# Kernel tuning notes

Measured on AMD Instinct MI355X. Metric: run time of the kernel, lower is better.

## Reference

```python
import jax, jax.numpy as jnp
import numpy as np

DIM = 1024
N_HEADS = 16
HEAD_DIM = 64
SEQ = 2048
BATCH = 2


def setup_inputs() -> dict:
    key = jax.random.key(0)
    ks = jax.random.split(key, 7)
    scale = 1.0 / np.sqrt(DIM)
    return {
        "q": jax.random.normal(ks[0], (BATCH, SEQ, DIM), dtype=jnp.float32),
        "k": jax.random.normal(ks[1], (BATCH, SEQ, DIM), dtype=jnp.float32),
        "v": jax.random.normal(ks[2], (BATCH, SEQ, DIM), dtype=jnp.float32),
        "wq": jax.random.normal(ks[3], (DIM, DIM), dtype=jnp.float32) * scale,
        "wk": jax.random.normal(ks[4], (DIM, DIM), dtype=jnp.float32) * scale,
        "wv": jax.random.normal(ks[5], (DIM, DIM), dtype=jnp.float32) * scale,
        "wo": jax.random.normal(ks[6], (DIM, DIM), dtype=jnp.float32) * scale,
    }


def reference(q, k, v, wq, wk, wv, wo):
    B, S, D = q.shape
    # Linear layers: y = x @ W.T (torch nn.Linear convention)
    qh = (q @ wq.T).reshape(B, S, N_HEADS, HEAD_DIM).transpose(0, 2, 1, 3)  # [B,H,S,hd]
    kh = (k @ wk.T).reshape(B, S, N_HEADS, HEAD_DIM).transpose(0, 2, 1, 3)
    vh = (v @ wv.T).reshape(B, S, N_HEADS, HEAD_DIM).transpose(0, 2, 1, 3)
    score = jnp.einsum('bhqd,bhkd->bhqk', qh, kh) / jnp.sqrt(jnp.float32(HEAD_DIM))
    # causal mask: upper triangle (j > i) set to -inf
    causal = jnp.tril(jnp.ones((S, S), dtype=bool))
    score = jnp.where(causal[None, None], score, -jnp.inf)
    attn = jax.nn.softmax(score, axis=-1)
    out = jnp.einsum('bhqk,bhkd->bhqd', attn, vh)  # [B,H,S,hd]
    out = out.transpose(0, 2, 1, 3).reshape(B, S, D)
    return out @ wo.T
```

## Files before the change

### kernel.cpp

```cpp
#include <hip/hip_runtime.h>

typedef unsigned short u16;
typedef unsigned int   u32;
typedef __bf16 bf16x8 __attribute__((ext_vector_type(8)));
typedef float  f32x4  __attribute__((ext_vector_type(4)));
typedef unsigned short u16x4 __attribute__((ext_vector_type(4)));
typedef unsigned short u16x8 __attribute__((ext_vector_type(8)));
typedef unsigned int   u32x2 __attribute__((ext_vector_type(2)));
typedef unsigned int   u32x4 __attribute__((ext_vector_type(4)));

#define DIM   1024
#define SEQ   2048
#define NH    16
#define HD    64
#define NBATCH 2

#define NEG_INF (-__builtin_inff())


__device__ __forceinline__ u16 f2bf(float f) {
  unsigned u = __float_as_uint(f);
  unsigned r = (u + 0x7FFFu + ((u >> 16) & 1u)) >> 16;
  return (u16)r;
}

__device__ __forceinline__ void gload16(const void* g, void* lds_uniform) {
  __builtin_amdgcn_global_load_lds(
      (__attribute__((address_space(1))) void*)(size_t)g,
      (__attribute__((address_space(3))) void*)lds_uniform,
      16, 0, 0);
}


__global__ __launch_bounds__(256) void cvt_all(
    const float* __restrict__ q, const float* __restrict__ k, const float* __restrict__ v,
    const float* __restrict__ wq, const float* __restrict__ wk, const float* __restrict__ wv,
    const float* __restrict__ wo, u16* __restrict__ ws) {
  const size_t M = 1u << 20;
  int b = blockIdx.x;
  const float* src;
  u16* dst;
  int idx;
  if (b < 6144) {
    int t = b >> 11; idx = b & 2047;
    src = (t == 0) ? q : (t == 1) ? k : v;
    dst = ws + (size_t)t * 4 * M;
  } else {
    int t = (b - 6144) >> 9; idx = (b - 6144) & 511;
    src = (t == 0) ? wq : (t == 1) ? wk : (t == 2) ? wv : wo;
    dst = ws + (12 + (size_t)t) * M;
  }
  size_t i = ((size_t)idx * 256 + threadIdx.x) * 8;
  float4 a = *(const float4*)(src + i);
  float4 c = *(const float4*)(src + i + 4);
  u16x8 o;
  o[0] = f2bf(a.x); o[1] = f2bf(a.y); o[2] = f2bf(a.z); o[3] = f2bf(a.w);
  o[4] = f2bf(c.x); o[5] = f2bf(c.y); o[6] = f2bf(c.z); o[7] = f2bf(c.w);
  *(u16x8*)(dst + i) = o;
}


__device__ __forceinline__ void gemm128_core(const u16* __restrict__ A,
                                             const u16* __restrict__ W,
                                             int bm, int bn,
                                             u16* lds, f32x4 (&acc)[4][4]) {
  const int K = 1024;
  const int tid = threadIdx.x;
  const int wave = tid >> 6, lane = tid & 63;
  const int quad = lane >> 4, l15 = lane & 15;
  const int warp_m = wave >> 1, warp_n = wave & 1;

  const int c0 = wave * 128 + lane, c1 = c0 + 64;
  const u16* Ag0 = A + (size_t)(bm * 128 + (c0 >> 2)) * K + (c0 & 3) * 8;
  const u16* Ag1 = A + (size_t)(bm * 128 + (c1 >> 2)) * K + (c1 & 3) * 8;
  const u16* Wg0 = W + (size_t)(bn * 128 + (c0 >> 2)) * K + (c0 & 3) * 8;
  const u16* Wg1 = W + (size_t)(bn * 128 + (c1 >> 2)) * K + (c1 & 3) * 8;
  const int lA0 = (wave * 2 + 0) * 512;
  const int lA1 = (wave * 2 + 1) * 512;
  const int lB0 = 4096 + (wave * 2 + 0) * 512;
  const int lB1 = 4096 + (wave * 2 + 1) * 512;

  gload16(Ag0, lds + lA0);
  gload16(Ag1, lds + lA1);
  gload16(Wg0, lds + lB0);
  gload16(Wg1, lds + lB1);

  for (int k0 = 0; k0 < K; k0 += 32) {
    const int buf = (k0 >> 5) & 1;
    u16* cur = lds + buf * 8192;
    __syncthreads();
    if (k0 + 32 < K) {
      u16* nxt = lds + (buf ^ 1) * 8192;
      gload16(Ag0 + k0 + 32, nxt + lA0);
      gload16(Ag1 + k0 + 32, nxt + lA1);
      gload16(Wg0 + k0 + 32, nxt + lB0);
      gload16(Wg1 + k0 + 32, nxt + lB1);
    }

    bf16x8 af[4], bfr[4];
#pragma unroll
    for (int i = 0; i < 4; ++i) {
      af[i]  = *(const bf16x8*)(cur + (warp_m * 64 + i * 16 + l15) * 32 + quad * 8);
      bfr[i] = *(const bf16x8*)(cur + 4096 + (warp_n * 64 + i * 16 + l15) * 32 + quad * 8);
    }
#pragma unroll
    for (int i = 0; i < 4; ++i)
#pragma unroll
      for (int j = 0; j < 4; ++j)
        acc[i][j] = __builtin_amdgcn_mfma_f32_16x16x32_bf16(af[i], bfr[j], acc[i][j], 0, 0, 0);
  }
}

__global__ __launch_bounds__(256) void gemm_qkv(
    const u16* __restrict__ qb, const u16* __restrict__ kb, const u16* __restrict__ vb,
    const u16* __restrict__ wq, const u16* __restrict__ wk, const u16* __restrict__ wv,
    u16* __restrict__ Qo, u16* __restrict__ Ko, u16* __restrict__ Vt) {
  __shared__ __align__(16) u16 lds[2][8192];
  const int id = blockIdx.x;
  const int c = id & 7, bn = (id >> 3) & 7, t = id >> 6;
  const int g = c + 8 * t;
  const int bm = g & 31, z = g >> 5;

  const u16* A = (z == 0) ? qb : (z == 1) ? kb : vb;
  const u16* W = (z == 0) ? wq : (z == 1) ? wk : wv;
  f32x4 acc[4][4] = {};
  gemm128_core(A, W, bm, bn, &lds[0][0], acc);

  const int tid = threadIdx.x;
  const int wave = tid >> 6, lane = tid & 63;
  const int quad = lane >> 4, l15 = lane & 15;
  const int warp_m = wave >> 1, warp_n = wave & 1;
#pragma unroll
  for (int i = 0; i < 4; ++i)
#pragma unroll
    for (int j = 0; j < 4; ++j) {
      int s0 = bm * 128 + warp_m * 64 + i * 16 + quad * 4;
      int n  = bn * 128 + warp_n * 64 + j * 16 + l15;
      int bb = s0 >> 11, sl0 = s0 & 2047, h = n >> 6, d = n & 63;
      if (z == 2) {
        int ssw = (sl0 & ~63) | ((((sl0 >> 3) & 7) ^ (d & 7)) << 3) | (sl0 & 7);
        u16x4 pv;
        pv[0] = f2bf(acc[i][j][0]); pv[1] = f2bf(acc[i][j][1]);
        pv[2] = f2bf(acc[i][j][2]); pv[3] = f2bf(acc[i][j][3]);
        *(u16x4*)(Vt + ((size_t)(bb * NH + h) * HD + d) * SEQ + ssw) = pv;
      } else if (z == 1) {
#pragma unroll
        for (int r = 0; r < 4; ++r) {
          int s = sl0 + r;
          int dsw = (((d >> 3) ^ (s & 7)) << 3) | (d & 7);
          Ko[((size_t)(bb * NH + h) * SEQ + s) * HD + dsw] = f2bf(acc[i][j][r]);
        }
      } else {
#pragma unroll
        for (int r = 0; r < 4; ++r)
          Qo[((size_t)(bb * NH + h) * SEQ + sl0 + r) * HD + d] = f2bf(acc[i][j][r] * 0.125f);
      }
    }
}

__global__ __launch_bounds__(256) void gemm_out(
    const u16* __restrict__ A, const u16* __restrict__ W, float* __restrict__ Out) {
  __shared__ __align__(16) u16 lds[2][8192];
  const int id = blockIdx.x;
  const int bn = (id >> 3) & 7;
  const int bm = (id & 7) + 8 * (id >> 6);
  f32x4 acc[4][4] = {};
  gemm128_core(A, W, bm, bn, &lds[0][0], acc);

  const int tid = threadIdx.x;
  const int wave = tid >> 6, lane = tid & 63;
  const int quad = lane >> 4, l15 = lane & 15;
  const int warp_m = wave >> 1, warp_n = wave & 1;
#pragma unroll
  for (int i = 0; i < 4; ++i)
#pragma unroll
    for (int j = 0; j < 4; ++j)
#pragma unroll
      for (int r = 0; r < 4; ++r) {
        int m = bm * 128 + warp_m * 64 + i * 16 + quad * 4 + r;
        int n = bn * 128 + warp_n * 64 + j * 16 + l15;
        Out[(size_t)m * DIM + n] = acc[i][j][r];
      }
}


__global__ __launch_bounds__(256) void attn_kernel(
    const u16* __restrict__ Q, const u16* __restrict__ K,
    const u16* __restrict__ Vt, u16* __restrict__ O) {
  __shared__ __align__(16) u16 Kl[2][4096];
  __shared__ __align__(16) u16 Vl[2][4096];
  __shared__ __align__(16) u32 Plm[4][16 * 36];

  const int tid = threadIdx.x;
  const int wave = tid >> 6, lane = tid & 63;
  const int quad = lane >> 4, l15 = lane & 15;
  const int bx = blockIdx.x;
  const int bh = bx & 31;
  const int qt = 31 - (bx >> 5);
  const int b = bh >> 4, h = bh & 15;

  const u16* qbase = Q + ((size_t)bh * SEQ + qt * 64 + wave * 16 + l15) * HD + quad * 8;
  const bf16x8 qf0 = *(const bf16x8*)(qbase);
  const bf16x8 qf1 = *(const bf16x8*)(qbase + 32);

  f32x4 o[4] = {};
  float l_sum = 0.f, m_run = NEG_INF;

  const int c0 = wave * 128 + lane, c1 = c0 + 64;
  const u16* Ksrc = K + (size_t)bh * SEQ * HD;
  const u16* Vsrc = Vt + (size_t)bh * HD * SEQ;
  const int sw0 = ((quad ^ (l15 & 7)) << 3);
  const int sw1 = (((4 + quad) ^ (l15 & 7)) << 3);

  {
    gload16(Ksrc + (size_t)c0 * 8, &Kl[0][(wave * 2 + 0) * 512]);
    gload16(Ksrc + (size_t)c1 * 8, &Kl[0][(wave * 2 + 1) * 512]);
    gload16(Vsrc + (size_t)(c0 >> 3) * SEQ + (c0 & 7) * 8, &Vl[0][(wave * 2 + 0) * 512]);
    gload16(Vsrc + (size_t)(c1 >> 3) * SEQ + (c1 & 7) * 8, &Vl[0][(wave * 2 + 1) * 512]);
  }

  u32* prow = &Plm[wave][l15 * 36];

  for (int kt = 0; kt <= qt; ++kt) {
    const int buf = kt & 1;
    __syncthreads();
    if (kt < qt) {
      const int nb = buf ^ 1;
      const size_t kb = (size_t)(kt + 1) * 64;
      gload16(Ksrc + (kb * HD) + (size_t)c0 * 8, &Kl[nb][(wave * 2 + 0) * 512]);
      gload16(Ksrc + (kb * HD) + (size_t)c1 * 8, &Kl[nb][(wave * 2 + 1) * 512]);
      gload16(Vsrc + (size_t)(c0 >> 3) * SEQ + kb + (c0 & 7) * 8, &Vl[nb][(wave * 2 + 0) * 512]);
      gload16(Vsrc + (size_t)(c1 >> 3) * SEQ + kb + (c1 & 7) * 8, &Vl[nb][(wave * 2 + 1) * 512]);
    }

    f32x4 s[4];
#pragma unroll
    for (int kn = 0; kn < 4; ++kn) {
      const u16* arow = &Kl[buf][(kn * 16 + l15) * 64];
      bf16x8 kf0 = *(const bf16x8*)(arow + sw0);
      bf16x8 kf1 = *(const bf16x8*)(arow + sw1);
      f32x4 z = {};
      z = __builtin_amdgcn_mfma_f32_16x16x32_bf16(kf0, qf0, z, 0, 0, 0);
      z = __builtin_amdgcn_mfma_f32_16x16x32_bf16(kf1, qf1, z, 0, 0, 0);
      s[kn] = z;
    }

    if (kt == qt) {
      const int qloc = wave * 16 + l15;
#pragma unroll
      for (int kn = 0; kn < 4; ++kn)
#pragma unroll
        for (int r = 0; r < 4; ++r)
          if (kn * 16 + quad * 4 + r > qloc) s[kn][r] = NEG_INF;
    }

    float mr = NEG_INF;
#pragma unroll
    for (int kn = 0; kn < 4; ++kn)
#pragma unroll
      for (int r = 0; r < 4; ++r) mr = fmaxf(mr, s[kn][r]);
    mr = fmaxf(mr, __shfl_xor(mr, 16));
    mr = fmaxf(mr, __shfl_xor(mr, 32));
    const float mnew = fmaxf(m_run, mr);
    const float alpha = __expf(m_run - mnew);
    m_run = mnew;
    float rs = 0.f;
#pragma unroll
    for (int kn = 0; kn < 4; ++kn)
#pragma unroll
      for (int r = 0; r < 4; ++r) {
        float p = __expf(s[kn][r] - mnew);
        s[kn][r] = p;
        rs += p;
      }
    rs += __shfl_xor(rs, 16);
    rs += __shfl_xor(rs, 32);
    l_sum = l_sum * alpha + rs;

    float aT[4];
#pragma unroll
    for (int r = 0; r < 4; ++r) aT[r] = __shfl(alpha, quad * 4 + r);
#pragma unroll
    for (int n = 0; n < 4; ++n)
#pragma unroll
      for (int r = 0; r < 4; ++r) o[n][r] *= aT[r];

#pragma unroll
    for (int kn = 0; kn < 4; ++kn) {
      u32x2 w;
      w[0] = (u32)f2bf(s[kn][0]) | ((u32)f2bf(s[kn][1]) << 16);
      w[1] = (u32)f2bf(s[kn][2]) | ((u32)f2bf(s[kn][3]) << 16);
      *(u32x2*)(prow + kn * 8 + quad * 2) = w;
    }
    u32x4 t0 = *(const u32x4*)(prow + quad * 4);
    u32x4 t1 = *(const u32x4*)(prow + 16 + quad * 4);
    bf16x8 pf0 = __builtin_bit_cast(bf16x8, t0);
    bf16x8 pf1 = __builtin_bit_cast(bf16x8, t1);

#pragma unroll
    for (int n = 0; n < 4; ++n) {
      const u16* vrow = &Vl[buf][(n * 16 + l15) * 64];
      bf16x8 vf0 = *(const bf16x8*)(vrow + sw0);
      bf16x8 vf1 = *(const bf16x8*)(vrow + sw1);
      o[n] = __builtin_amdgcn_mfma_f32_16x16x32_bf16(pf0, vf0, o[n], 0, 0, 0);
      o[n] = __builtin_amdgcn_mfma_f32_16x16x32_bf16(pf1, vf1, o[n], 0, 0, 0);
    }
  }

  float inv = 1.f / l_sum;
  float iT[4];
#pragma unroll
  for (int r = 0; r < 4; ++r) iT[r] = __shfl(inv, quad * 4 + r);
#pragma unroll
  for (int r = 0; r < 4; ++r) {
    int srow = qt * 64 + wave * 16 + quad * 4 + r;
#pragma unroll
    for (int n = 0; n < 4; ++n) {
      int col = h * HD + n * 16 + l15;
      O[((size_t)b * SEQ + srow) * DIM + col] = f2bf(o[n][r] * iT[r]);
    }
  }
}


extern "C" void kernel_launch(void* const* d_in, const int* in_sizes, int n_in,
                              void* d_out, int out_size, void* d_ws, size_t ws_size,
                              hipStream_t stream) {
  (void)in_sizes; (void)n_in; (void)out_size; (void)ws_size;
  const float* q  = (const float*)d_in[0];
  const float* k  = (const float*)d_in[1];
  const float* v  = (const float*)d_in[2];
  const float* wq = (const float*)d_in[3];
  const float* wk = (const float*)d_in[4];
  const float* wv = (const float*)d_in[5];
  const float* wo = (const float*)d_in[6];

  u16* ws = (u16*)d_ws;
  const size_t EL = 1u << 20;
  u16* QB = ws + 0 * EL;
  u16* KB = ws + 4 * EL;
  u16* VB = ws + 8 * EL;
  u16* WQ = ws + 12 * EL;
  u16* WK = ws + 13 * EL;
  u16* WV = ws + 14 * EL;
  u16* WO = ws + 15 * EL;
  u16* Qw = ws + 16 * EL;
  u16* Kw = ws + 20 * EL;
  u16* Vtw = ws + 24 * EL;
  u16* AO = ws + 28 * EL;

  cvt_all<<<8192, 256, 0, stream>>>(q, k, v, wq, wk, wv, wo, ws);
  gemm_qkv<<<768, 256, 0, stream>>>(QB, KB, VB, WQ, WK, WV, Qw, Kw, Vtw);
  attn_kernel<<<1024, 256, 0, stream>>>(Qw, Kw, Vtw, AO);
  gemm_out<<<256, 256, 0, stream>>>(AO, WO, (float*)d_out);
}
```

Measured before the change: 203.2 us.

## Use exp2 softmax with folded log2e, transposed PV MFMA, swizzled P staging

Folds log2(e) into the Q scale so the softmax can use the native exp2 instruction instead of __expf. Swaps the MFMA operand order for P·V so the output accumulator is laid out per query row. This removes the alpha and inverse-sum shuffles and allows packed 8-byte output stores. The P staging buffer gets an XOR swizzle instead of padding, and bf16 packing uses the hardware cvt_pk instruction when it is available. Together these cut VALU, shuffle and LDS-conflict overhead in the attention inner loop. The cost is a more intricate layout that has to stay consistent with the MFMA fragment mapping.

```diff
diff --git a/kernel.cpp b/kernel.cpp
--- a/kernel.cpp
+++ b/kernel.cpp
@@ -16,12 +16,23 @@
 #define NBATCH 2
 
 #define NEG_INF (-__builtin_inff())
+#define QSCALE 0.1803368801111204f
 
 
 __device__ __forceinline__ u16 f2bf(float f) {
   unsigned u = __float_as_uint(f);
   unsigned r = (u + 0x7FFFu + ((u >> 16) & 1u)) >> 16;
   return (u16)r;
+}
+
+__device__ __forceinline__ u32 pkbf(float a, float b) {
+#if __has_builtin(__builtin_amdgcn_cvt_pk_bf16_f32)
+  typedef __bf16 bf16x2 __attribute__((ext_vector_type(2)));
+  bf16x2 t = __builtin_amdgcn_cvt_pk_bf16_f32(a, b);
+  return __builtin_bit_cast(u32, t);
+#else
+  return (u32)f2bf(a) | ((u32)f2bf(b) << 16);
+#endif
 }
 
 __device__ __forceinline__ void gload16(const void* g, void* lds_uniform) {
@@ -153,7 +164,7 @@
       } else {
 #pragma unroll
         for (int r = 0; r < 4; ++r)
-          Qo[((size_t)(bb * NH + h) * SEQ + sl0 + r) * HD + d] = f2bf(acc[i][j][r] * 0.125f);
+          Qo[((size_t)(bb * NH + h) * SEQ + sl0 + r) * HD + d] = f2bf(acc[i][j][r] * QSCALE);
       }
     }
 }
@@ -189,8 +200,7 @@
     const u16* __restrict__ Vt, u16* __restrict__ O) {
   __shared__ __align__(16) u16 Kl[2][4096];
   __shared__ __align__(16) u16 Vl[2][4096];
-  __shared__ __align__(16) u32 Plm[4][16 * 36];
-
+  __shared__ __align__(16) u32 Plm[4][512];
   const int tid = threadIdx.x;
   const int wave = tid >> 6, lane = tid & 63;
   const int quad = lane >> 4, l15 = lane & 15;
@@ -219,7 +229,9 @@
     gload16(Vsrc + (size_t)(c1 >> 3) * SEQ + (c1 & 7) * 8, &Vl[0][(wave * 2 + 1) * 512]);
   }
 
-  u32* prow = &Plm[wave][l15 * 36];
+  u32* prow = &Plm[wave][l15 * 32];
+  const int psw = l15 & 7;
+  const int phalf = (quad & 1) * 2, pbhi = quad >> 1;
 
   for (int kt = 0; kt <= qt; ++kt) {
     const int buf = kt & 1;
@@ -262,14 +274,14 @@
     mr = fmaxf(mr, __shfl_xor(mr, 16));
     mr = fmaxf(mr, __shfl_xor(mr, 32));
     const float mnew = fmaxf(m_run, mr);
-    const float alpha = __expf(m_run - mnew);
+    const float alpha = __builtin_amdgcn_exp2f(m_run - mnew);
     m_run = mnew;
     float rs = 0.f;
 #pragma unroll
     for (int kn = 0; kn < 4; ++kn)
 #pragma unroll
       for (int r = 0; r < 4; ++r) {
-        float p = __expf(s[kn][r] - mnew);
+        float p = __builtin_amdgcn_exp2f(s[kn][r] - mnew);
         s[kn][r] = p;
         rs += p;
       }
@@ -277,23 +289,20 @@
     rs += __shfl_xor(rs, 32);
     l_sum = l_sum * alpha + rs;
 
-    float aT[4];
-#pragma unroll
-    for (int r = 0; r < 4; ++r) aT[r] = __shfl(alpha, quad * 4 + r);
 #pragma unroll
     for (int n = 0; n < 4; ++n)
 #pragma unroll
-      for (int r = 0; r < 4; ++r) o[n][r] *= aT[r];
+      for (int r = 0; r < 4; ++r) o[n][r] *= alpha;
 
 #pragma unroll
     for (int kn = 0; kn < 4; ++kn) {
       u32x2 w;
-      w[0] = (u32)f2bf(s[kn][0]) | ((u32)f2bf(s[kn][1]) << 16);
-      w[1] = (u32)f2bf(s[kn][2]) | ((u32)f2bf(s[kn][3]) << 16);
-      *(u32x2*)(prow + kn * 8 + quad * 2) = w;
-    }
-    u32x4 t0 = *(const u32x4*)(prow + quad * 4);
-    u32x4 t1 = *(const u32x4*)(prow + 16 + quad * 4);
+      w[0] = pkbf(s[kn][0], s[kn][1]);
+      w[1] = pkbf(s[kn][2], s[kn][3]);
+      *(u32x2*)(prow + (((2 * kn + pbhi) ^ psw) << 2) + phalf) = w;
+    }
+    u32x4 t0 = *(const u32x4*)(prow + ((quad ^ psw) << 2));
+    u32x4 t1 = *(const u32x4*)(prow + (((4 + quad) ^ psw) << 2));
     bf16x8 pf0 = __builtin_bit_cast(bf16x8, t0);
     bf16x8 pf1 = __builtin_bit_cast(bf16x8, t1);
 
@@ -302,23 +311,20 @@
       const u16* vrow = &Vl[buf][(n * 16 + l15) * 64];
       bf16x8 vf0 = *(const bf16x8*)(vrow + sw0);
       bf16x8 vf1 = *(const bf16x8*)(vrow + sw1);
-      o[n] = __builtin_amdgcn_mfma_f32_16x16x32_bf16(pf0, vf0, o[n], 0, 0, 0);
-      o[n] = __builtin_amdgcn_mfma_f32_16x16x32_bf16(pf1, vf1, o[n], 0, 0, 0);
-    }
-  }
-
-  float inv = 1.f / l_sum;
-  float iT[4];
-#pragma unroll
-  for (int r = 0; r < 4; ++r) iT[r] = __shfl(inv, quad * 4 + r);
-#pragma unroll
-  for (int r = 0; r < 4; ++r) {
-    int srow = qt * 64 + wave * 16 + quad * 4 + r;
-#pragma unroll
-    for (int n = 0; n < 4; ++n) {
-      int col = h * HD + n * 16 + l15;
-      O[((size_t)b * SEQ + srow) * DIM + col] = f2bf(o[n][r] * iT[r]);
-    }
+      o[n] = __builtin_amdgcn_mfma_f32_16x16x32_bf16(vf0, pf0, o[n], 0, 0, 0);
+      o[n] = __builtin_amdgcn_mfma_f32_16x16x32_bf16(vf1, pf1, o[n], 0, 0, 0);
+    }
+  }
+
+  const float inv = 1.f / l_sum;
+  const int srow = qt * 64 + wave * 16 + l15;
+  u16* obase = O + ((size_t)b * SEQ + srow) * DIM + h * HD + quad * 4;
+#pragma unroll
+  for (int n = 0; n < 4; ++n) {
+    u32x2 st;
+    st[0] = pkbf(o[n][0] * inv, o[n][1] * inv);
+    st[1] = pkbf(o[n][2] * inv, o[n][3] * inv);
+    *(u32x2*)(obase + n * 16) = st;
   }
 }
 
```

Measured after the change: 202.4 us. No clear change (-0.4%).
